# Kernel optimization log

Hardware: AMD Instinct MI355X
Metric: run time of the kernel (lower is better)

## Reference

```python
import jax, jax.numpy as jnp
import numpy as np

N = 200000
K = 64           # max_neighbors
DIM = 3
EPS_W = 1e-8     # weight regularizer
LAM = 1e-6       # normal-equation Tikhonov regularizer


def setup_inputs() -> dict:
    key = jax.random.key(0)
    k1, k2, k3 = jax.random.split(key, 3)
    coords = jax.random.normal(k1, (N, DIM), dtype=jnp.float32)
    neighbor_matrix = jax.random.randint(k2, (N, K), 0, N, dtype=jnp.int64)
    y = jax.random.normal(k3, (N, 1), dtype=jnp.float32)
    return {"coords": coords, "neighbor_matrix": neighbor_matrix, "y": y}


def reference(coords, neighbor_matrix, y):
    # Batched least-squares first derivative (FirstDeriv._forward_batched).
    valid = (neighbor_matrix != -1)[..., None].astype(coords.dtype)  # [N, K, 1]
    # gather neighbor coords/values, form masked differences
    dv = (coords[neighbor_matrix] - coords[:, None, :]) * valid      # [N, K, DIM]
    du = (y[neighbor_matrix] - y[:, None, :]) * valid                # [N, K, 1]
    # inverse-distance-squared weights
    w = 1.0 / (jnp.einsum('bni,bni->bn', dv, dv) + EPS_W)            # [N, K]
    # per-node normal equations A x = B (A: [N, DIM, DIM], B: [N, DIM, 1])
    A = jnp.einsum('bni,bn,bnj->bij', dv, w, dv)
    B = jnp.einsum('bni,bn,bnk->bik', dv, w, du)
    A_reg = A + LAM * jnp.eye(DIM, dtype=A.dtype)
    grad_u = jnp.linalg.solve(A_reg, B)                              # [N, DIM, 1]
    # original returns [grad_u[:, [i]] for i in range(dim)]; we return them
    # concatenated as one [N, DIM] array (identical values).
    return grad_u[..., 0]
```

## Files before the change

kernel.cpp:

```cpp
#include <hip/hip_runtime.h>

#define NN 200000
#define KK 64
#define EPS_W 1e-8f
#define LAM 1e-6

__global__ __launch_bounds__(256) void pack_kernel(
    const float* __restrict__ coords,
    const float* __restrict__ y,
    float4* __restrict__ packed)
{
    const int i = blockIdx.x * 256 + threadIdx.x;
    if (i < NN) {
        packed[i] = make_float4(coords[3 * i + 0],
                                coords[3 * i + 1],
                                coords[3 * i + 2],
                                y[i]);
    }
}

__global__ __launch_bounds__(256) void fd_kernel(
    const int4* __restrict__ nbr4,
    const float4* __restrict__ packed,
    float* __restrict__ out)
{
    const int tid  = threadIdx.x;
    const int sub  = tid & 7;
    const int node = blockIdx.x * 32 + (tid >> 3);

    const float4 c = packed[node];

    const int4 ia = nbr4[node * 16 + sub * 2 + 0];
    const int4 ib = nbr4[node * 16 + sub * 2 + 1];

    float4 p[8];
    p[0] = packed[ia.x]; p[1] = packed[ia.y];
    p[2] = packed[ia.z]; p[3] = packed[ia.w];
    p[4] = packed[ib.x]; p[5] = packed[ib.y];
    p[6] = packed[ib.z]; p[7] = packed[ib.w];

    float sxx = 0.f, sxy = 0.f, sxz = 0.f;
    float syy = 0.f, syz = 0.f, szz = 0.f;
    float bx = 0.f, by = 0.f, bz = 0.f;

    #pragma unroll
    for (int i = 0; i < 8; ++i) {
        const float dx = p[i].x - c.x;
        const float dy = p[i].y - c.y;
        const float dz = p[i].z - c.z;
        const float du = p[i].w - c.w;
        const float w  = 1.0f / (dx * dx + dy * dy + dz * dz + EPS_W);
        const float wdx = w * dx, wdy = w * dy, wdz = w * dz;
        sxx += wdx * dx; sxy += wdx * dy; sxz += wdx * dz;
        syy += wdy * dy; syz += wdy * dz; szz += wdz * dz;
        bx  += wdx * du; by  += wdy * du; bz  += wdz * du;
    }

    #pragma unroll
    for (int off = 1; off <= 4; off <<= 1) {
        sxx += __shfl_xor(sxx, off);
        sxy += __shfl_xor(sxy, off);
        sxz += __shfl_xor(sxz, off);
        syy += __shfl_xor(syy, off);
        syz += __shfl_xor(syz, off);
        szz += __shfl_xor(szz, off);
        bx  += __shfl_xor(bx, off);
        by  += __shfl_xor(by, off);
        bz  += __shfl_xor(bz, off);
    }

    if (sub == 0) {
        const double a00 = (double)sxx + LAM;
        const double a01 = (double)sxy;
        const double a02 = (double)sxz;
        const double a11 = (double)syy + LAM;
        const double a12 = (double)syz;
        const double a22 = (double)szz + LAM;

        const double c00 = a11 * a22 - a12 * a12;
        const double c01 = a02 * a12 - a01 * a22;
        const double c02 = a01 * a12 - a02 * a11;
        const double det = a00 * c00 + a01 * c01 + a02 * c02;
        const double inv = 1.0 / det;

        const double i00 = c00 * inv;
        const double i01 = c01 * inv;
        const double i02 = c02 * inv;
        const double i11 = (a00 * a22 - a02 * a02) * inv;
        const double i12 = (a01 * a02 - a00 * a12) * inv;
        const double i22 = (a00 * a11 - a01 * a01) * inv;

        out[node * 3 + 0] = (float)(i00 * bx + i01 * by + i02 * bz);
        out[node * 3 + 1] = (float)(i01 * bx + i11 * by + i12 * bz);
        out[node * 3 + 2] = (float)(i02 * bx + i12 * by + i22 * bz);
    }
}

extern "C" void kernel_launch(void* const* d_in, const int* in_sizes, int n_in,
                              void* d_out, int out_size, void* d_ws, size_t ws_size,
                              hipStream_t stream) {
    const float* coords = (const float*)d_in[0];
    const int*   nbr    = (const int*)d_in[1];
    const float* y      = (const float*)d_in[2];
    float*       out    = (float*)d_out;
    float4*      packed = (float4*)d_ws;

    pack_kernel<<<(NN + 255) / 256, 256, 0, stream>>>(coords, y, packed);

    const int grid = NN / 32;
    fd_kernel<<<grid, 256, 0, stream>>>((const int4*)nbr, packed, out);
}
```

Before: 138.0 us.

## Use four threads per node with sixteen gathers each and nontemporal loads

Halves the threads per node so each thread gathers sixteen neighbor records instead of eight, and interleaves the neighbor-index loads across the four threads. Marks the neighbor gathers as nontemporal and adds an occupancy hint to the launch bounds. The aim is more memory-level parallelism per thread and fewer shuffle reductions, at the cost of higher register use. The nontemporal hint may reduce cache reuse of the packed node array.

```diff
diff --git a/kernel.cpp b/kernel.cpp
--- a/kernel.cpp
+++ b/kernel.cpp
@@ -5,46 +5,55 @@
 #define EPS_W 1e-8f
 #define LAM 1e-6
 
+typedef float v4f __attribute__((ext_vector_type(4)));
+
 __global__ __launch_bounds__(256) void pack_kernel(
     const float* __restrict__ coords,
     const float* __restrict__ y,
-    float4* __restrict__ packed)
+    v4f* __restrict__ packed)
 {
     const int i = blockIdx.x * 256 + threadIdx.x;
     if (i < NN) {
-        packed[i] = make_float4(coords[3 * i + 0],
-                                coords[3 * i + 1],
-                                coords[3 * i + 2],
-                                y[i]);
+        v4f p;
+        p.x = coords[3 * i + 0];
+        p.y = coords[3 * i + 1];
+        p.z = coords[3 * i + 2];
+        p.w = y[i];
+        packed[i] = p;
     }
 }
 
-__global__ __launch_bounds__(256) void fd_kernel(
+__global__ __launch_bounds__(256, 4) void fd_kernel(
     const int4* __restrict__ nbr4,
-    const float4* __restrict__ packed,
+    const v4f* __restrict__ packed,
     float* __restrict__ out)
 {
     const int tid  = threadIdx.x;
-    const int sub  = tid & 7;
-    const int node = blockIdx.x * 32 + (tid >> 3);
+    const int sub  = tid & 3;
+    const int node = blockIdx.x * 64 + (tid >> 2);
 
-    const float4 c = packed[node];
+    const v4f c = packed[node];
 
-    const int4 ia = nbr4[node * 16 + sub * 2 + 0];
-    const int4 ib = nbr4[node * 16 + sub * 2 + 1];
+    int4 iv[4];
+    #pragma unroll
+    for (int k = 0; k < 4; ++k)
+        iv[k] = nbr4[node * 16 + sub + 4 * k];
 
-    float4 p[8];
-    p[0] = packed[ia.x]; p[1] = packed[ia.y];
-    p[2] = packed[ia.z]; p[3] = packed[ia.w];
-    p[4] = packed[ib.x]; p[5] = packed[ib.y];
-    p[6] = packed[ib.z]; p[7] = packed[ib.w];
+    v4f p[16];
+    #pragma unroll
+    for (int k = 0; k < 4; ++k) {
+        p[4 * k + 0] = __builtin_nontemporal_load(&packed[iv[k].x]);
+        p[4 * k + 1] = __builtin_nontemporal_load(&packed[iv[k].y]);
+        p[4 * k + 2] = __builtin_nontemporal_load(&packed[iv[k].z]);
+        p[4 * k + 3] = __builtin_nontemporal_load(&packed[iv[k].w]);
+    }
 
     float sxx = 0.f, sxy = 0.f, sxz = 0.f;
     float syy = 0.f, syz = 0.f, szz = 0.f;
     float bx = 0.f, by = 0.f, bz = 0.f;
 
     #pragma unroll
-    for (int i = 0; i < 8; ++i) {
+    for (int i = 0; i < 16; ++i) {
         const float dx = p[i].x - c.x;
         const float dy = p[i].y - c.y;
         const float dz = p[i].z - c.z;
@@ -57,7 +66,7 @@
     }
 
     #pragma unroll
-    for (int off = 1; off <= 4; off <<= 1) {
+    for (int off = 1; off <= 2; off <<= 1) {
         sxx += __shfl_xor(sxx, off);
         sxy += __shfl_xor(sxy, off);
         sxz += __shfl_xor(sxz, off);
@@ -103,10 +112,10 @@
     const int*   nbr    = (const int*)d_in[1];
     const float* y      = (const float*)d_in[2];
     float*       out    = (float*)d_out;
-    float4*      packed = (float4*)d_ws;
+    v4f*         packed = (v4f*)d_ws;
 
     pack_kernel<<<(NN + 255) / 256, 256, 0, stream>>>(coords, y, packed);
 
-    const int grid = NN / 32;
+    const int grid = NN / 64;
     fd_kernel<<<grid, 256, 0, stream>>>((const int4*)nbr, packed, out);
 }
```

After: 248.6 us. 80.1% more time.
